# Optimization experiments

Measured on AMD Instinct MI355X. Metric: run time of the kernel, lower is better.

## Reference

```python
import jax, jax.numpy as jnp
import numpy as np

INIT_STD = 0.002
DEFAULT_BETA = 1.0 / np.sqrt(64.0)  # 1/sqrt(head_dim)


def setup_inputs() -> dict:
    key = jax.random.key(0)
    k1, k2, k3 = jax.random.split(key, 3)
    B, S, E = 4, 2048, 768
    H, D = 12, 64
    x = jax.random.normal(k1, (B, S, E), dtype=jnp.float32)
    q_proj_weight = INIT_STD * jax.random.normal(k2, (H, D, E), dtype=jnp.float32)
    k_proj_weight = INIT_STD * jax.random.normal(k3, (H, D, E), dtype=jnp.float32)
    beta = jnp.full((H,), DEFAULT_BETA, dtype=jnp.float32)
    return {"x": x, "q_proj_weight": q_proj_weight, "k_proj_weight": k_proj_weight, "beta": beta}


def reference(x, q_proj_weight, k_proj_weight, beta):
    # x: [B,S,E]; W^{Q,K}: [H,D,E]; beta: [H]
    q = jnp.einsum("bse,hde->bshd", x, q_proj_weight)  # [B,S,H,D]
    k = jnp.einsum("bse,hde->bshd", x, k_proj_weight)  # [B,S,H,D]
    # scores[b,h,s,t] = beta_h * <Q_{bsh}, K_{bth}>
    scores = jnp.einsum("bshd,bthd,h->bhst", q, k, beta)
    S = x.shape[1]
    diag = jnp.eye(S, dtype=bool)  # self-exclusion mask (B != C)
    scores = jnp.where(diag[None, None, :, :], -jnp.inf, scores)
    lse = jax.nn.logsumexp(scores, axis=-1)  # [B,H,S]
    # E = -sum_{b,h,s} (1/beta_h) * logsumexp_t
    energy = -jnp.sum(lse / beta[None, :, None])
    return energy
```

## Files before the change

kernel.cpp:

```cpp
#include <hip/hip_runtime.h>
#include <hip/hip_bf16.h>

typedef __attribute__((ext_vector_type(8))) short short8v;
typedef __attribute__((ext_vector_type(4))) float f32x4;

static constexpr int B_ = 4, S_ = 2048, E_ = 768, H_ = 12, D_ = 64;
static constexpr int NROWS = B_ * H_ * S_;
static constexpr float LOG2E = 1.44269504088896340736f;
static constexpr float LN2 = 0.69314718055994530942f;

typedef __attribute__((address_space(3))) unsigned int lds_u32;
typedef const __attribute__((address_space(1))) unsigned int glb_u32;

__device__ __forceinline__ void gload16(const void* g, void* l) {
  __builtin_amdgcn_global_load_lds((glb_u32*)g, (lds_u32*)l, 16, 0, 0);
}

#define VM0 asm volatile("s_waitcnt vmcnt(0)" ::: "memory")
#define VM2 asm volatile("s_waitcnt vmcnt(2)" ::: "memory")
#define BAR __builtin_amdgcn_s_barrier()

__device__ __forceinline__ unsigned short f2bf(float f) {
  union { float f; unsigned int u; } v; v.f = f;
  unsigned int u = v.u;
  unsigned int r = (u + 0x7fffu + ((u >> 16) & 1u)) >> 16;
  return (unsigned short)r;
}

__global__ __launch_bounds__(256) void cvt_x_kernel(const float4* __restrict__ x,
                                                    ushort4* __restrict__ xb, int n4) {
  int i = blockIdx.x * 256 + threadIdx.x;
  if (i >= n4) return;
  float4 v = x[i];
  ushort4 o;
  o.x = f2bf(v.x); o.y = f2bf(v.y); o.z = f2bf(v.z); o.w = f2bf(v.w);
  xb[i] = o;
}

__global__ __launch_bounds__(256) void cvt_w_kernel(const float4* __restrict__ wq,
                                                    const float4* __restrict__ wk,
                                                    const float* __restrict__ beta,
                                                    ushort4* __restrict__ wb, int n4) {
  int i = blockIdx.x * 256 + threadIdx.x;
  if (i < n4) {
    int row = i / (E_ / 4);
    float sc = beta[row >> 6] * LOG2E;
    float4 v = wq[i];
    ushort4 o;
    o.x = f2bf(v.x * sc); o.y = f2bf(v.y * sc); o.z = f2bf(v.z * sc); o.w = f2bf(v.w * sc);
    wb[i] = o;
  } else if (i < 2 * n4) {
    int j = i - n4;
    float4 v = wk[j];
    ushort4 o;
    o.x = f2bf(v.x); o.y = f2bf(v.y); o.z = f2bf(v.z); o.w = f2bf(v.w);
    wb[i] = o;
  }
}

__global__ __launch_bounds__(256) void proj_kernel(const unsigned short* __restrict__ xb,
                                                   const unsigned short* __restrict__ wb,
                                                   unsigned short* __restrict__ Qb,
                                                   unsigned short* __restrict__ Kb) {
  __shared__ unsigned short lA[128 * 32];
  __shared__ unsigned short lB[128 * 32];
  const int mt = blockIdx.x, nt = blockIdx.y;
  const int t = threadIdx.x;
  const int wid = t >> 6, lane = t & 63, l15 = lane & 15, lhi = lane >> 4;
  const int wr = (wid >> 1) * 64, wc = (wid & 1) * 64;

  f32x4 acc[4][4] = {};

  const int row = t >> 2, ch = t & 3;
  const unsigned short* gA = xb + (size_t)(mt * 128 + row) * E_ + ch * 8;
  const unsigned short* gB = wb + (size_t)(nt * 128 + row) * E_ + ch * 8;

  for (int k0 = 0; k0 < E_; k0 += 32) {
    gload16(gA + k0, &lA[t * 8]);
    gload16(gA + (size_t)64 * E_ + k0, &lA[2048 + t * 8]);
    gload16(gB + k0, &lB[t * 8]);
    gload16(gB + (size_t)64 * E_ + k0, &lB[2048 + t * 8]);
    __syncthreads();
    short8v aF[4], bF[4];
#pragma unroll
    for (int m = 0; m < 4; ++m)
      aF[m] = *(const short8v*)&lA[(wr + m * 16 + l15) * 32 + lhi * 8];
#pragma unroll
    for (int n = 0; n < 4; ++n)
      bF[n] = *(const short8v*)&lB[(wc + n * 16 + l15) * 32 + lhi * 8];
#pragma unroll
    for (int m = 0; m < 4; ++m)
#pragma unroll
      for (int n = 0; n < 4; ++n)
        acc[m][n] = __builtin_amdgcn_mfma_f32_16x16x32_bf16(aF[m], bF[n], acc[m][n], 0, 0, 0);
    __syncthreads();
  }

  const int nbase = nt * 128 + wc;
  unsigned short* dst = (nbase < 768) ? Qb : Kb;
  const int nb = (nbase < 768) ? nbase : nbase - 768;
#pragma unroll
  for (int m = 0; m < 4; ++m)
#pragma unroll
    for (int n = 0; n < 4; ++n)
#pragma unroll
      for (int r = 0; r < 4; ++r) {
        int M = mt * 128 + wr + m * 16 + lhi * 4 + r;
        int col = nb + n * 16 + l15;
        int h = col >> 6, d = col & 63;
        int b = M >> 11, s = M & (S_ - 1);
        dst[((((size_t)b * H_ + h) * S_ + s) << 6) + d] = f2bf(acc[m][n][r]);
      }
}

__device__ __forceinline__ void stageK(const unsigned short* __restrict__ Kbase, int t0,
                                       int tid, unsigned short* lbuf) {
  const int w = tid >> 6;
  const int r = tid >> 3;
  const int c = (tid & 7) ^ (r & 7);
  const char* src = (const char*)Kbase + ((size_t)(t0 + r) << 7) + (c << 4);
  char* ldst = (char*)lbuf + (w << 10);
  gload16(src, ldst);
  gload16(src + (32 << 7), ldst + 4096);
}

__device__ __forceinline__ void computeTile64(const unsigned short* lbuf, const short8v q[4][2],
                                              f32x4 sp[4], bool isD, int l15, int lhi) {
  short8v kf[4][2];
  const int sw = l15 & 7;
#pragma unroll
  for (int f = 0; f < 4; ++f) {
    const char* p = (const char*)lbuf + ((f * 16 + l15) << 7);
    kf[f][0] = *(const short8v*)(p + ((lhi ^ sw) << 4));
    kf[f][1] = *(const short8v*)(p + (((lhi + 4) ^ sw) << 4));
  }
#pragma unroll
  for (int rb = 0; rb < 4; ++rb) {
    f32x4 acc[4] = {};
#pragma unroll
    for (int f = 0; f < 4; ++f) {
      acc[f] = __builtin_amdgcn_mfma_f32_16x16x32_bf16(q[rb][0], kf[f][0], acc[f], 0, 0, 0);
      acc[f] = __builtin_amdgcn_mfma_f32_16x16x32_bf16(q[rb][1], kf[f][1], acc[f], 0, 0, 0);
    }
#pragma unroll
    for (int f = 0; f < 4; ++f) {
      f32x4 e;
#pragma unroll
      for (int r = 0; r < 4; ++r) e[r] = __builtin_amdgcn_exp2f(acc[f][r]);
      if (isD && f == rb) {
#pragma unroll
        for (int r = 0; r < 4; ++r)
          if (l15 == lhi * 4 + r) e[r] = 0.f;
      }
      sp[rb] += e;
    }
  }
}

__global__ __launch_bounds__(256) void lse_kernel(const unsigned short* __restrict__ Qb,
                                                  const unsigned short* __restrict__ Kb,
                                                  float* __restrict__ rowsum) {
  __shared__ __align__(16) unsigned short lK[3][4096];
  const int L = blockIdx.x + 8 * (blockIdx.y + 12 * blockIdx.z);
  const int xcd = L & 7, j = L >> 3;
  const int split = j & 3;
  const int st = (j >> 2) & 7;
  const int g = xcd + 8 * (j >> 5);
  const int h = g % H_, b = g / H_;

  const int tid = threadIdx.x;
  const int wid = tid >> 6, lane = tid & 63;
  const int l15 = lane & 15, lhi = lane >> 4;
  const size_t hb = ((size_t)b * H_ + h) * S_;
  const unsigned short* Qbase = Qb + hb * D_;
  const unsigned short* Kbase = Kb + hb * D_;
  const int s0 = st * 256 + wid * 64;
  const int tb = split * 512;

  short8v q[4][2];
#pragma unroll
  for (int rb = 0; rb < 4; ++rb) {
    const unsigned short* qr = Qbase + (size_t)(s0 + rb * 16 + l15) * D_ + lhi * 8;
    q[rb][0] = *(const short8v*)qr;
    q[rb][1] = *(const short8v*)(qr + 32);
  }

  const int dtile = ((s0 >> 9) == split) ? ((s0 - tb) >> 6) : -1;

  f32x4 sp[4] = {};
  stageK(Kbase, tb, tid, lK[0]);
  stageK(Kbase, tb + 64, tid, lK[1]);
  int bi = 0;
#pragma unroll 1
  for (int i = 0; i < 7; ++i) {
    VM2;
    BAR;
    if (i < 6) {
      int bs_ = bi + 2; if (bs_ >= 3) bs_ -= 3;
      stageK(Kbase, tb + (i + 2) * 64, tid, lK[bs_]);
    }
    computeTile64(lK[bi], q, sp, i == dtile, l15, lhi);
    if (++bi == 3) bi = 0;
  }
  VM0; BAR;
  computeTile64(lK[bi], q, sp, 7 == dtile, l15, lhi);

#pragma unroll
  for (int rb = 0; rb < 4; ++rb)
#pragma unroll
    for (int r = 0; r < 4; ++r) {
      float s = sp[rb][r];
#pragma unroll
      for (int off = 1; off < 16; off <<= 1) s += __shfl_xor(s, off, 64);
      if (l15 == 0)
        rowsum[(size_t)split * NROWS + hb + s0 + rb * 16 + lhi * 4 + r] = s;
    }
}

__global__ __launch_bounds__(256) void finish1_kernel(const float* __restrict__ rowsum,
                                                      const float* __restrict__ beta,
                                                      float* __restrict__ partial) {
  int row = blockIdx.x * 256 + threadIdx.x;
  float s = (rowsum[row] + rowsum[NROWS + row]) +
            (rowsum[2 * NROWS + row] + rowsum[3 * NROWS + row]);
  int h = (row >> 11) % H_;
  float c = __builtin_amdgcn_logf(s) * LN2 / beta[h];
#pragma unroll
  for (int off = 1; off < 64; off <<= 1) c += __shfl_xor(c, off, 64);
  __shared__ float wsum[4];
  int wid = threadIdx.x >> 6;
  if ((threadIdx.x & 63) == 0) wsum[wid] = c;
  __syncthreads();
  if (threadIdx.x == 0) partial[blockIdx.x] = wsum[0] + wsum[1] + wsum[2] + wsum[3];
}

__global__ __launch_bounds__(256) void finish2_kernel(const float* __restrict__ partial, int n,
                                                      float* __restrict__ out) {
  float s = 0.f;
  for (int i = threadIdx.x; i < n; i += 256) s += partial[i];
#pragma unroll
  for (int off = 1; off < 64; off <<= 1) s += __shfl_xor(s, off, 64);
  __shared__ float wsum[4];
  int wid = threadIdx.x >> 6;
  if ((threadIdx.x & 63) == 0) wsum[wid] = s;
  __syncthreads();
  if (threadIdx.x == 0) out[0] = -(wsum[0] + wsum[1] + wsum[2] + wsum[3]);
}

extern "C" void kernel_launch(void* const* d_in, const int* in_sizes, int n_in,
                              void* d_out, int out_size, void* d_ws, size_t ws_size,
                              hipStream_t stream) {
  const float* x    = (const float*)d_in[0];
  const float* wq   = (const float*)d_in[1];
  const float* wk   = (const float*)d_in[2];
  const float* beta = (const float*)d_in[3];

  char* ws = (char*)d_ws;
  const size_t xb_bytes = (size_t)B_ * S_ * E_ * 2;
  const size_t wb_bytes = (size_t)2 * H_ * D_ * E_ * 2;
  const size_t qk_bytes = (size_t)B_ * H_ * S_ * D_ * 2;
  const size_t rs_bytes = (size_t)4 * NROWS * 4;
  unsigned short* xb = (unsigned short*)ws;
  unsigned short* wb = (unsigned short*)(ws + xb_bytes);
  unsigned short* Qb = (unsigned short*)(ws + xb_bytes + wb_bytes);
  unsigned short* Kb = (unsigned short*)(ws + xb_bytes + wb_bytes + qk_bytes);
  float* rowsum      = (float*)(ws + xb_bytes + wb_bytes + 2 * qk_bytes);
  float* partial     = (float*)(ws + xb_bytes + wb_bytes + 2 * qk_bytes + rs_bytes);

  int nx4 = (B_ * S_ * E_) / 4;
  cvt_x_kernel<<<(nx4 + 255) / 256, 256, 0, stream>>>((const float4*)x, (ushort4*)xb, nx4);

  int nw4 = (H_ * D_ * E_) / 4;
  cvt_w_kernel<<<(2 * nw4 + 255) / 256, 256, 0, stream>>>((const float4*)wq, (const float4*)wk,
                                                          beta, (ushort4*)wb, nw4);

  dim3 pgrid((B_ * S_) / 128, (2 * H_ * D_) / 128);
  proj_kernel<<<pgrid, 256, 0, stream>>>(xb, wb, Qb, Kb);

  dim3 lgrid(S_ / 256, H_, B_ * 4);
  lse_kernel<<<lgrid, 256, 0, stream>>>(Qb, Kb, rowsum);

  finish1_kernel<<<NROWS / 256, 256, 0, stream>>>(rowsum, beta, partial);
  finish2_kernel<<<1, 256, 0, stream>>>(partial, NROWS / 256, (float*)d_out);
}
```

Before: 79.66 us.

## Fuse fp32-to-bf16 conversion of x into projection GEMM tile loads

```diff
diff --git a/kernel.cpp b/kernel.cpp
--- a/kernel.cpp
+++ b/kernel.cpp
@@ -25,16 +25,6 @@
   unsigned int u = v.u;
   unsigned int r = (u + 0x7fffu + ((u >> 16) & 1u)) >> 16;
   return (unsigned short)r;
-}
-
-__global__ __launch_bounds__(256) void cvt_x_kernel(const float4* __restrict__ x,
-                                                    ushort4* __restrict__ xb, int n4) {
-  int i = blockIdx.x * 256 + threadIdx.x;
-  if (i >= n4) return;
-  float4 v = x[i];
-  ushort4 o;
-  o.x = f2bf(v.x); o.y = f2bf(v.y); o.z = f2bf(v.z); o.w = f2bf(v.w);
-  xb[i] = o;
 }
 
 __global__ __launch_bounds__(256) void cvt_w_kernel(const float4* __restrict__ wq,
@@ -58,11 +48,11 @@
   }
 }
 
-__global__ __launch_bounds__(256) void proj_kernel(const unsigned short* __restrict__ xb,
+__global__ __launch_bounds__(256) void proj_kernel(const float* __restrict__ x,
                                                    const unsigned short* __restrict__ wb,
                                                    unsigned short* __restrict__ Qb,
                                                    unsigned short* __restrict__ Kb) {
-  __shared__ unsigned short lA[128 * 32];
+  __shared__ float lAf[128 * 32];
   __shared__ unsigned short lB[128 * 32];
   const int mt = blockIdx.x, nt = blockIdx.y;
   const int t = threadIdx.x;
@@ -71,20 +61,36 @@
 
   f32x4 acc[4][4] = {};
 
+  const int r3 = t >> 3;
+  const int cs = (t & 7) ^ (r3 & 7);
+  const float* gA = x + (size_t)(mt * 128 + r3) * E_ + cs * 4;
+
   const int row = t >> 2, ch = t & 3;
-  const unsigned short* gA = xb + (size_t)(mt * 128 + row) * E_ + ch * 8;
   const unsigned short* gB = wb + (size_t)(nt * 128 + row) * E_ + ch * 8;
 
   for (int k0 = 0; k0 < E_; k0 += 32) {
-    gload16(gA + k0, &lA[t * 8]);
-    gload16(gA + (size_t)64 * E_ + k0, &lA[2048 + t * 8]);
-    gload16(gB + k0, &lB[t * 8]);
+    gload16(gA + k0,                (char*)lAf + t * 16);
+    gload16(gA + 32 * E_ + k0,      (char*)lAf + 4096 + t * 16);
+    gload16(gA + 64 * E_ + k0,      (char*)lAf + 8192 + t * 16);
+    gload16(gA + 96 * E_ + k0,      (char*)lAf + 12288 + t * 16);
+    gload16(gB + k0,                &lB[t * 8]);
     gload16(gB + (size_t)64 * E_ + k0, &lB[2048 + t * 8]);
     __syncthreads();
     short8v aF[4], bF[4];
-#pragma unroll
-    for (int m = 0; m < 4; ++m)
-      aF[m] = *(const short8v*)&lA[(wr + m * 16 + l15) * 32 + lhi * 8];
+    const int sw_ = l15 & 7;
+#pragma unroll
+    for (int m = 0; m < 4; ++m) {
+      const int r = wr + m * 16 + l15;
+      const float* base = lAf + r * 32;
+      f32x4 u0 = *(const f32x4*)(base + ((((lhi << 1)    ) ^ sw_) << 2));
+      f32x4 u1 = *(const f32x4*)(base + ((((lhi << 1) | 1) ^ sw_) << 2));
+      union { short8v s8; unsigned int u[4]; } af;
+      asm("v_cvt_pk_bf16_f32 %0, %1, %2" : "=v"(af.u[0]) : "v"(u0[0]), "v"(u0[1]));
+      asm("v_cvt_pk_bf16_f32 %0, %1, %2" : "=v"(af.u[1]) : "v"(u0[2]), "v"(u0[3]));
+      asm("v_cvt_pk_bf16_f32 %0, %1, %2" : "=v"(af.u[2]) : "v"(u1[0]), "v"(u1[1]));
+      asm("v_cvt_pk_bf16_f32 %0, %1, %2" : "=v"(af.u[3]) : "v"(u1[2]), "v"(u1[3]));
+      aF[m] = af.s8;
+    }
 #pragma unroll
     for (int n = 0; n < 4; ++n)
       bF[n] = *(const short8v*)&lB[(wc + n * 16 + l15) * 32 + lhi * 8];
@@ -256,26 +262,21 @@
   const float* beta = (const float*)d_in[3];
 
   char* ws = (char*)d_ws;
-  const size_t xb_bytes = (size_t)B_ * S_ * E_ * 2;
   const size_t wb_bytes = (size_t)2 * H_ * D_ * E_ * 2;
   const size_t qk_bytes = (size_t)B_ * H_ * S_ * D_ * 2;
   const size_t rs_bytes = (size_t)4 * NROWS * 4;
-  unsigned short* xb = (unsigned short*)ws;
-  unsigned short* wb = (unsigned short*)(ws + xb_bytes);
-  unsigned short* Qb = (unsigned short*)(ws + xb_bytes + wb_bytes);
-  unsigned short* Kb = (unsigned short*)(ws + xb_bytes + wb_bytes + qk_bytes);
-  float* rowsum      = (float*)(ws + xb_bytes + wb_bytes + 2 * qk_bytes);
-  float* partial     = (float*)(ws + xb_bytes + wb_bytes + 2 * qk_bytes + rs_bytes);
-
-  int nx4 = (B_ * S_ * E_) / 4;
-  cvt_x_kernel<<<(nx4 + 255) / 256, 256, 0, stream>>>((const float4*)x, (ushort4*)xb, nx4);
+  unsigned short* wb = (unsigned short*)ws;
+  unsigned short* Qb = (unsigned short*)(ws + wb_bytes);
+  unsigned short* Kb = (unsigned short*)(ws + wb_bytes + qk_bytes);
+  float* rowsum      = (float*)(ws + wb_bytes + 2 * qk_bytes);
+  float* partial     = (float*)(ws + wb_bytes + 2 * qk_bytes + rs_bytes);
 
   int nw4 = (H_ * D_ * E_) / 4;
   cvt_w_kernel<<<(2 * nw4 + 255) / 256, 256, 0, stream>>>((const float4*)wq, (const float4*)wk,
                                                           beta, (ushort4*)wb, nw4);
 
   dim3 pgrid((B_ * S_) / 128, (2 * H_ * D_) / 128);
-  proj_kernel<<<pgrid, 256, 0, stream>>>(xb, wb, Qb, Kb);
+  proj_kernel<<<pgrid, 256, 0, stream>>>(x, wb, Qb, Kb);
 
   dim3 lgrid(S_ / 256, H_, B_ * 4);
   lse_kernel<<<lgrid, 256, 0, stream>>>(Qb, Kb, rowsum);
```

After: 77.92 us. 1.02x faster.
